# Optimization experiments

Measured on AMD Instinct MI355X. Metric: run time of the kernel, lower is better.

## Reference

```python
import jax, jax.numpy as jnp
import numpy as np
from jax import lax

CHANNELS = 3
SCALE = 0.25
SIGMA = (1.0 / SCALE - 1.0) / 2.0          # 1.5
KSIZE = 2 * round(SIGMA * 4) + 1           # 13
KA = KSIZE // 2                            # 6 (symmetric since KSIZE odd)
KB = KA


def _gaussian_kernel():
    # separable 2D gaussian, normalized to sum 1, shape [K, K, 1, C] (HWIO, depthwise)
    r = jnp.arange(KSIZE, dtype=jnp.float32)
    mean = (KSIZE - 1) / 2.0
    g1d = jnp.exp(-((r - mean) ** 2) / (2.0 * SIGMA ** 2))
    k2d = g1d[:, None] * g1d[None, :]
    k2d = k2d / jnp.sum(k2d)
    return jnp.tile(k2d[:, :, None, None], (1, 1, 1, CHANNELS))


def setup_inputs() -> dict:
    key = jax.random.key(0)
    x = jax.random.normal(key, (32, 512, 512, CHANNELS), dtype=jnp.float32)
    return {"x": x}


def reference(x) -> jnp.ndarray:
    N, H, W, C = x.shape
    kernel = _gaussian_kernel()
    # depthwise gaussian blur; symmetric (ka, kb) zero padding + VALID == SAME output size
    blurred = lax.conv_general_dilated(
        x, kernel,
        window_strides=(1, 1),
        padding=((KA, KB), (KA, KB)),
        dimension_numbers=("NHWC", "HWIO", "NHWC"),
        feature_group_count=C,
    )
    # nearest-neighbor downsample: src = min(floor(dst * in/out), in-1)
    y_max = int(H * SCALE)
    x_max = int(W * SCALE)
    ys = jnp.minimum(jnp.floor(jnp.arange(y_max, dtype=jnp.float32) * (H / y_max)), H - 1).astype(jnp.int32)
    xs = jnp.minimum(jnp.floor(jnp.arange(x_max, dtype=jnp.float32) * (W / x_max)), W - 1).astype(jnp.int32)
    return blurred[:, ys][:, :, xs]  # [N, y_max, x_max, C]
```

## Files before the change

### kernel.cpp

```cpp
#include <hip/hip_runtime.h>
#include <math.h>


namespace {
constexpr int N_IMG    = 32;
constexpr int H_IN     = 512;
constexpr int W_IN     = 512;
constexpr int C_CH     = 3;
constexpr int H_OUT    = 128;
constexpr int W_OUT    = 128;
constexpr int T_ROWS   = 8;
constexpr int BANDS    = H_OUT / T_ROWS;
constexpr int PITCH    = 532;
constexpr int ROW_ELEMS = W_IN * C_CH;
constexpr int NTHREADS = 384;
constexpr int LDS_FLOATS = 2 * 4 * 3 * PITCH;
}

__global__ __launch_bounds__(NTHREADS, 3)
void aa_blur_down(const float* __restrict__ in, float* __restrict__ out) {
  __shared__ __align__(16) float lds[LDS_FLOATS];

  const int tid = threadIdx.x;
  const int j   = tid / 3;
  const int c   = tid % 3;
  const int n    = blockIdx.x / BANDS;
  const int band = blockIdx.x % BANDS;
  const int i0   = band * T_ROWS;

  float wt[13];
  {
    float s = 0.f;
#pragma unroll
    for (int r = 0; r < 13; ++r) {
      const float d = (float)r - 6.0f;
      wt[r] = expf(-d * d * (1.0f / 4.5f));
      s += wt[r];
    }
    const float inv = 1.0f / s;
#pragma unroll
    for (int r = 0; r < 13; ++r) wt[r] *= inv;
  }

  const int qstart = i0 - 2;
  const int qend   = i0 + T_ROWS;
  const float* img = in + (size_t)n * H_IN * ROW_ELEMS;

  for (int idx = tid; idx < LDS_FLOATS; idx += NTHREADS) lds[idx] = 0.f;
  __syncthreads();

  float4 pre4[4];

  auto load_quad = [&](int q) {
#pragma unroll
    for (int m = 0; m < 4; ++m) {
      const int y = 4 * q + m;
      if (y >= 0 && y < H_IN) {
        pre4[m] = reinterpret_cast<const float4*>(img + (size_t)y * ROW_ELEMS)[tid];
      } else {
        pre4[m] = make_float4(0.f, 0.f, 0.f, 0.f);
      }
    }
  };

  const int c0 = tid % 3;
  const int x0 = (4 * tid) / 3;
  auto store_quad = [&](int b) {
#pragma unroll
    for (int m = 0; m < 4; ++m) {
      const int rowbase = (b * 4 + m) * 3 * PITCH;
      float v0 = pre4[m].x, v1 = pre4[m].y, v2 = pre4[m].z, v3 = pre4[m].w;
#pragma unroll
      for (int e = 0; e < 4; ++e) {
        const int ce = c0 + e;
        const int cc = (ce >= 3) ? ce - 3 : ce;
        const int xx = x0 + ((ce >= 3) ? 1 : 0);
        const float v = (e == 0) ? v0 : (e == 1) ? v1 : (e == 2) ? v2 : v3;
        lds[rowbase + cc * PITCH + xx + 8] = v;
      }
    }
  };

  load_quad(qstart);
  store_quad(0);
  __syncthreads();

  float A0 = 0.f, A1 = 0.f, A2 = 0.f, A3 = 0.f;

  for (int q = qstart; q <= qend; ++q) {
    const int b = (q - qstart) & 1;
    const bool more = (q < qend);
    if (more) load_quad(q + 1);

    float h[4];
#pragma unroll
    for (int p = 0; p < 4; ++p) {
      const float4* plane4 =
          reinterpret_cast<const float4*>(&lds[((b * 4 + p) * 3 + c) * PITCH + 4 * j]);
      const float4 wa = plane4[0];
      const float4 wb = plane4[1];
      const float4 wc = plane4[2];
      const float4 wd = plane4[3];
      float hh;
      hh = wt[0] * wa.z;
      hh = fmaf(wt[1],  wa.w, hh);
      hh = fmaf(wt[2],  wb.x, hh);
      hh = fmaf(wt[3],  wb.y, hh);
      hh = fmaf(wt[4],  wb.z, hh);
      hh = fmaf(wt[5],  wb.w, hh);
      hh = fmaf(wt[6],  wc.x, hh);
      hh = fmaf(wt[7],  wc.y, hh);
      hh = fmaf(wt[8],  wc.z, hh);
      hh = fmaf(wt[9],  wc.w, hh);
      hh = fmaf(wt[10], wd.x, hh);
      hh = fmaf(wt[11], wd.y, hh);
      hh = fmaf(wt[12], wd.z, hh);
      h[p] = hh;
    }

    A0 = fmaf(wt[10], h[0], A0); A0 = fmaf(wt[11], h[1], A0); A0 = fmaf(wt[12], h[2], A0);
    A1 = fmaf(wt[6],  h[0], A1); A1 = fmaf(wt[7],  h[1], A1); A1 = fmaf(wt[8],  h[2], A1); A1 = fmaf(wt[9], h[3], A1);
    A2 = fmaf(wt[2],  h[0], A2); A2 = fmaf(wt[3],  h[1], A2); A2 = fmaf(wt[4],  h[2], A2); A2 = fmaf(wt[5], h[3], A2);
    A3 = fmaf(wt[0],  h[2], A3); A3 = fmaf(wt[1],  h[3], A3);

    const int i_out = q - 1;
    if (i_out >= i0) {
      out[(size_t)(n * H_OUT + i_out) * (W_OUT * C_CH) + tid] = A0;
    }
    A0 = A1; A1 = A2; A2 = A3; A3 = 0.f;

    if (more) store_quad(b ^ 1);
    __syncthreads();
  }
}

extern "C" void kernel_launch(void* const* d_in, const int* in_sizes, int n_in,
                              void* d_out, int out_size, void* d_ws, size_t ws_size,
                              hipStream_t stream) {
  const float* x = (const float*)d_in[0];
  float* out = (float*)d_out;
  (void)in_sizes; (void)n_in; (void)out_size; (void)d_ws; (void)ws_size;
  hipLaunchKernelGGL(aa_blur_down, dim3(N_IMG * BANDS), dim3(NTHREADS), 0, stream, x, out);
}
```

Measured before the change: 153.6 us.

## Apply vertical blur in registers before horizontal pass, shrinking LDS staging

Swaps the separable filter order. The vertical 13-tap pass now runs directly on global-memory float4 rows held in registers, using a triple-buffered register prefetch and a fully unrolled 11-step loop that skips dead rows. Only one vertically blurred row is staged through a small double-buffered LDS buffer for the horizontal pass, which removes the per-quad LDS scatter of four input rows. It also cuts LDS usage by a factor of four, but raises register pressure, so the launch-bounds occupancy hint drops from 3 to 2.

After: 146.7 us. 1.05x faster.

```diff
diff --git a/kernel.cpp b/kernel.cpp
--- a/kernel.cpp
+++ b/kernel.cpp
@@ -3,21 +3,26 @@
 
 
 namespace {
-constexpr int N_IMG    = 32;
-constexpr int H_IN     = 512;
-constexpr int W_IN     = 512;
-constexpr int C_CH     = 3;
-constexpr int H_OUT    = 128;
-constexpr int W_OUT    = 128;
-constexpr int T_ROWS   = 8;
-constexpr int BANDS    = H_OUT / T_ROWS;
-constexpr int PITCH    = 532;
+constexpr int N_IMG   = 32;
+constexpr int H_IN    = 512;
+constexpr int W_IN    = 512;
+constexpr int C_CH    = 3;
+constexpr int H_OUT   = 128;
+constexpr int W_OUT   = 128;
+constexpr int T_ROWS  = 8;
+constexpr int BANDS   = H_OUT / T_ROWS;
+constexpr int PITCH   = 532;
 constexpr int ROW_ELEMS = W_IN * C_CH;
 constexpr int NTHREADS = 384;
-constexpr int LDS_FLOATS = 2 * 4 * 3 * PITCH;
+constexpr int LDS_FLOATS = 2 * 3 * PITCH;
 }
 
-__global__ __launch_bounds__(NTHREADS, 3)
+__device__ __forceinline__ float4 f4fma(float w, const float4& p, const float4& a) {
+  return make_float4(fmaf(w, p.x, a.x), fmaf(w, p.y, a.y),
+                     fmaf(w, p.z, a.z), fmaf(w, p.w, a.w));
+}
+
+__global__ __launch_bounds__(NTHREADS, 2)
 void aa_blur_down(const float* __restrict__ in, float* __restrict__ out) {
   __shared__ __align__(16) float lds[LDS_FLOATS];
 
@@ -43,64 +48,69 @@
   }
 
   const int qstart = i0 - 2;
-  const int qend   = i0 + T_ROWS;
   const float* img = in + (size_t)n * H_IN * ROW_ELEMS;
 
   for (int idx = tid; idx < LDS_FLOATS; idx += NTHREADS) lds[idx] = 0.f;
   __syncthreads();
 
-  float4 pre4[4];
+  int off_e[4];
+#pragma unroll
+  for (int e = 0; e < 4; ++e) {
+    const int ce = c + e;
+    const int cc = (ce >= 3) ? ce - 3 : ce;
+    const int xx = (4 * tid) / 3 + ((ce >= 3) ? 1 : 0);
+    off_e[e] = cc * PITCH + xx + 8;
+  }
 
-  auto load_quad = [&](int q) {
+  float4 P[3][4];
+  auto loadq = [&](int slot, int s) {
+    const int q = qstart + s;
 #pragma unroll
     for (int m = 0; m < 4; ++m) {
+      const bool dead = (s == 0 && m < 2) || (s == 10 && m == 3);
       const int y = 4 * q + m;
-      if (y >= 0 && y < H_IN) {
-        pre4[m] = reinterpret_cast<const float4*>(img + (size_t)y * ROW_ELEMS)[tid];
+      if (!dead && (unsigned)y < (unsigned)H_IN) {
+        P[slot][m] = reinterpret_cast<const float4*>(img + (size_t)y * ROW_ELEMS)[tid];
       } else {
-        pre4[m] = make_float4(0.f, 0.f, 0.f, 0.f);
+        P[slot][m] = make_float4(0.f, 0.f, 0.f, 0.f);
       }
     }
   };
 
-  const int c0 = tid % 3;
-  const int x0 = (4 * tid) / 3;
-  auto store_quad = [&](int b) {
+  float4 A0 = make_float4(0,0,0,0), A1 = A0, A2 = A0, A3 = A0;
+
+  loadq(0, 0);
+  loadq(1, 1);
+
 #pragma unroll
-    for (int m = 0; m < 4; ++m) {
-      const int rowbase = (b * 4 + m) * 3 * PITCH;
-      float v0 = pre4[m].x, v1 = pre4[m].y, v2 = pre4[m].z, v3 = pre4[m].w;
-#pragma unroll
-      for (int e = 0; e < 4; ++e) {
-        const int ce = c0 + e;
-        const int cc = (ce >= 3) ? ce - 3 : ce;
-        const int xx = x0 + ((ce >= 3) ? 1 : 0);
-        const float v = (e == 0) ? v0 : (e == 1) ? v1 : (e == 2) ? v2 : v3;
-        lds[rowbase + cc * PITCH + xx + 8] = v;
-      }
-    }
-  };
+  for (int s = 0; s <= 10; ++s) {
+    if (s + 2 <= 10) loadq((s + 2) % 3, s + 2);
 
-  load_quad(qstart);
-  store_quad(0);
-  __syncthreads();
+    const float4 p0 = P[s % 3][0];
+    const float4 p1 = P[s % 3][1];
+    const float4 p2 = P[s % 3][2];
+    const float4 p3 = P[s % 3][3];
 
-  float A0 = 0.f, A1 = 0.f, A2 = 0.f, A3 = 0.f;
+    if (s >= 3)           { A0 = f4fma(wt[10], p0, A0); A0 = f4fma(wt[11], p1, A0); A0 = f4fma(wt[12], p2, A0); }
+    if (s >= 2 && s <= 9) { A1 = f4fma(wt[6],  p0, A1); A1 = f4fma(wt[7],  p1, A1); A1 = f4fma(wt[8],  p2, A1); A1 = f4fma(wt[9], p3, A1); }
+    if (s >= 1 && s <= 8) { A2 = f4fma(wt[2],  p0, A2); A2 = f4fma(wt[3],  p1, A2); A2 = f4fma(wt[4],  p2, A2); A2 = f4fma(wt[5], p3, A2); }
+    if (s <= 7)           { A3 = f4fma(wt[0],  p2, A3); A3 = f4fma(wt[1],  p3, A3); }
 
-  for (int q = qstart; q <= qend; ++q) {
-    const int b = (q - qstart) & 1;
-    const bool more = (q < qend);
-    if (more) load_quad(q + 1);
+    if (s >= 3) {
+      const int i = i0 + s - 3;
+      const int b = (s - 3) & 1;
+      float* buf = &lds[b * 3 * PITCH];
+      buf[off_e[0]] = A0.x;
+      buf[off_e[1]] = A0.y;
+      buf[off_e[2]] = A0.z;
+      buf[off_e[3]] = A0.w;
+      __syncthreads();
 
-    float h[4];
-#pragma unroll
-    for (int p = 0; p < 4; ++p) {
-      const float4* plane4 =
-          reinterpret_cast<const float4*>(&lds[((b * 4 + p) * 3 + c) * PITCH + 4 * j]);
-      const float4 wa = plane4[0];
-      const float4 wb = plane4[1];
-      const float4 wc = plane4[2];
-      const float4 wd = plane4[3];
+      const float4* pl = reinterpret_cast<const float4*>(&buf[c * PITCH + 4 * j]);
+      const float4 wa = pl[0];
+      const float4 wb = pl[1];
+      const float4 wc = pl[2];
+      const float4 wd = pl[3];
       float hh;
       hh = wt[0] * wa.z;
       hh = fmaf(wt[1],  wa.w, hh);
@@ -115,22 +125,10 @@
       hh = fmaf(wt[10], wd.x, hh);
       hh = fmaf(wt[11], wd.y, hh);
       hh = fmaf(wt[12], wd.z, hh);
-      h[p] = hh;
+      out[(size_t)(n * H_OUT + i) * (W_OUT * C_CH) + tid] = hh;
     }
 
-    A0 = fmaf(wt[10], h[0], A0); A0 = fmaf(wt[11], h[1], A0); A0 = fmaf(wt[12], h[2], A0);
-    A1 = fmaf(wt[6],  h[0], A1); A1 = fmaf(wt[7],  h[1], A1); A1 = fmaf(wt[8],  h[2], A1); A1 = fmaf(wt[9], h[3], A1);
-    A2 = fmaf(wt[2],  h[0], A2); A2 = fmaf(wt[3],  h[1], A2); A2 = fmaf(wt[4],  h[2], A2); A2 = fmaf(wt[5], h[3], A2);
-    A3 = fmaf(wt[0],  h[2], A3); A3 = fmaf(wt[1],  h[3], A3);
-
-    const int i_out = q - 1;
-    if (i_out >= i0) {
-      out[(size_t)(n * H_OUT + i_out) * (W_OUT * C_CH) + tid] = A0;
-    }
-    A0 = A1; A1 = A2; A2 = A3; A3 = 0.f;
-
-    if (more) store_quad(b ^ 1);
-    __syncthreads();
+    A0 = A1; A1 = A2; A2 = A3; A3 = make_float4(0.f, 0.f, 0.f, 0.f);
   }
 }
 
```
